# Kernel tuning notes

Measured on AMD Instinct MI355X. Metric: run time of the kernel, lower is better.

The kernel has to match this reference:

```python
import jax, jax.numpy as jnp
import numpy as np

PATCH = 96
VOL = 192
STRIDE = 48
C = 2
B = 1
GD = 48  # global low-res grid


def _gaussian_wt(p):
    # MONAI-style gaussian importance map: delta at center (p//2), sigma = 0.125*p,
    # separable gaussian product, normalized so max == 1.
    i = jnp.arange(p, dtype=jnp.float32)
    c = jnp.float32(p // 2)
    sigma = jnp.float32(0.125 * p)
    g = jnp.exp(-0.5 * ((i - c) / sigma) ** 2)
    w = g[:, None, None] * g[None, :, None] * g[None, None, :]  # [p,p,p]
    return w / w.max()


def setup_inputs() -> dict:
    key = jax.random.key(0)
    k1, k2 = jax.random.split(key)
    # deterministic overlapping patch grid (stride 48, patch 96, vol 192 -> 3 per axis)
    pos = list(range(0, VOL - PATCH + 1, STRIDE))
    starts = np.array([[d, h, w] for d in pos for h in pos for w in pos], dtype=np.int32)  # [27,3]
    K = starts.shape[0]
    patch_logits = jax.random.normal(k1, (K * B, C, PATCH, PATCH, PATCH), dtype=jnp.float32)
    global_logit = jax.random.normal(k2, (B, C, GD, GD, GD), dtype=jnp.float32)
    return {
        "patch_logits": patch_logits,
        "global_logit": global_logit,
        "patch_starts": jnp.asarray(starts),
    }


def reference(patch_logits, global_logit, patch_starts):
    K, Cc, P = patch_logits.shape[0], patch_logits.shape[1], patch_logits.shape[2]
    V = VOL
    wt = _gaussian_wt(P)  # [P,P,P], matches fixed_wt buffer

    offs = jnp.arange(P, dtype=jnp.int32)
    dd = patch_starts[:, 0][:, None] + offs  # [K,P]
    hh = patch_starts[:, 1][:, None] + offs
    ww = patch_starts[:, 2][:, None] + offs
    # flattened voxel index per patch element: [K,P,P,P]
    flat = ((dd[:, :, None, None] * V + hh[:, None, :, None]) * V + ww[:, None, None, :]).reshape(-1)

    # weighted scatter-add of all patches (batch=1 so all patches target batch 0)
    vals = (patch_logits * wt[None, None]).transpose(1, 0, 2, 3, 4).reshape(Cc, -1)  # [C, K*P^3]
    final = jnp.zeros((Cc, V * V * V), patch_logits.dtype).at[:, flat].add(vals)

    wvals = jnp.broadcast_to(wt, (K, P, P, P)).reshape(-1)
    wmap = jnp.full((V * V * V,), 1e-20, patch_logits.dtype).at[flat].add(wvals)
    mask = jnp.zeros((V * V * V,), patch_logits.dtype).at[flat].set(1.0)

    # trilinear upsample, align_corners=False (half-pixel) == jax.image.resize linear
    up = jax.image.resize(global_logit, (B, Cc, V, V, V), method='trilinear')

    out = (final / wmap).reshape(B, Cc, V, V, V)
    out = out + jnp.where(mask.reshape(B, 1, V, V, V) == 1.0, 0.0, up)
    return out
```

## Files before the change

### kernel.cpp

```cpp
#include <hip/hip_runtime.h>


constexpr int V  = 192;
constexpr int P  = 96;
constexpr int S  = 48;
constexpr int NC = 2;
constexpr int TH = 8;
constexpr int NT = 384;
constexpr int CF4 = TH * P / 4;
constexpr int NBLK = NC * V * (V / TH);

__global__ __launch_bounds__(NT) void
DynamicPatchAggregator_85418309583422_kernel(const float* __restrict__ patches,
                                             float* __restrict__ out)
{
    __shared__ __align__(16) float  sg[P];
    __shared__ __align__(16) float4 stage[12 * CF4];

    const int t = threadIdx.x;
    if (t < P) {
        float x = ((float)(t - 48)) * (1.0f / 12.0f);
        sg[t] = __expf(-0.5f * x * x);
    }

    const int bid = blockIdx.x;
    const int ht  = bid % (V / TH);
    const int d   = (bid / (V / TH)) % V;
    const int c   = bid / ((V / TH) * V);
    const int H0  = ht * TH;

    const int dq  = d / S;
    const int kd0 = max(0, dq - 1);
    const int nkd = (dq == 1 || dq == 2) ? 2 : 1;
    const int hq  = H0 / S;
    const int kh0 = max(0, hq - 1);
    const int nkh = (hq == 1 || hq == 2) ? 2 : 1;

    const int nchunk = nkd * nkh * 3;
    const int total  = nchunk * CF4;
    for (int base = t; base < total; base += 4 * NT) {
        float4 v[4];
        int   su[4];
        int nv = 0;
#pragma unroll
        for (int q = 0; q < 4; ++q) {
            const int u = base + q * NT;
            if (u < total) {
                const int chunk = u / CF4;
                const int r     = u % CF4;
                const int kw = chunk % 3;
                const int j  = (chunk / 3) % nkh;
                const int i  = chunk / (3 * nkh);
                const int kd = kd0 + i, kh = kh0 + j;
                const int pd  = d  - kd * S;
                const int ph0 = H0 - kh * S;
                const int k   = (kd * 3 + kh) * 3 + kw;
                const int off = (((k * NC + c) * P + pd) * P + ph0) * P;
                v[q]  = reinterpret_cast<const float4*>(patches + off)[r];
                su[q] = ((i * 2 + j) * 3 + kw) * CF4 + r;
                nv = q + 1;
            }
        }
#pragma unroll
        for (int q = 0; q < 4; ++q)
            if (q < nv) stage[su[q]] = v[q];
    }
    __syncthreads();

    const int hl = t / 48;
    const int w4 = t % 48;
    const int h  = H0 + hl;

    const int  wr  = w4 / 12;
    const int  kwa = max(0, wr - 1);
    const bool wv  = (wr == 1) | (wr == 2);
    const int  kwb = wv ? kwa + 1 : kwa;
    const int  pqa = w4 - kwa * 12;
    const int  pqb = wv ? pqa - 12 : pqa;
    const float4 gwa = reinterpret_cast<const float4*>(sg)[pqa];
    float4 gwb = reinterpret_cast<const float4*>(sg)[pqb];
    if (!wv) gwb = make_float4(0.0f, 0.0f, 0.0f, 0.0f);

    const float gd0 = sg[d - kd0 * S];
    const float gd1 = (nkd == 2) ? sg[d - (kd0 + 1) * S] : 0.0f;
    const float gh0 = sg[h - kh0 * S];
    const float gh1 = (nkh == 2) ? sg[h - (kh0 + 1) * S] : 0.0f;

    const float gdA[2] = {gd0, gd1};
    const float ghA[2] = {gh0, gh1};
    const int   iA[2]  = {0, nkd - 1};
    const int   jA[2]  = {0, nkh - 1};
    const int   kwA[2] = {kwa, kwb};
    const int   pqA[2] = {pqa, pqb};
    const float4 gwA[2] = {gwa, gwb};

    float4 acc = make_float4(0.0f, 0.0f, 0.0f, 0.0f);
#pragma unroll
    for (int i = 0; i < 2; ++i)
#pragma unroll
        for (int j = 0; j < 2; ++j) {
            const float a = gdA[i] * ghA[j];
#pragma unroll
            for (int k = 0; k < 2; ++k) {
                const float4 pv =
                    stage[((iA[i] * 2 + jA[j]) * 3 + kwA[k]) * CF4 + hl * 24 + pqA[k]];
                const float4 g = gwA[k];
                acc.x += (a * g.x) * pv.x;
                acc.y += (a * g.y) * pv.y;
                acc.z += (a * g.z) * pv.z;
                acc.w += (a * g.w) * pv.w;
            }
        }

    const float GdGh = (gd0 + gd1) * (gh0 + gh1);
    float4 o;
    o.x = acc.x / (GdGh * (gwa.x + gwb.x) + 1e-20f);
    o.y = acc.y / (GdGh * (gwa.y + gwb.y) + 1e-20f);
    o.z = acc.z / (GdGh * (gwa.z + gwb.z) + 1e-20f);
    o.w = acc.w / (GdGh * (gwa.w + gwb.w) + 1e-20f);

    reinterpret_cast<float4*>(out)[bid * NT + t] = o;
}

extern "C" void kernel_launch(void* const* d_in, const int* in_sizes, int n_in,
                              void* d_out, int out_size, void* d_ws, size_t ws_size,
                              hipStream_t stream) {
    const float* patches = (const float*)d_in[0];
    float* out = (float*)d_out;

    DynamicPatchAggregator_85418309583422_kernel<<<NBLK, NT, 0, stream>>>(patches, out);
}
```

Before: 309.6 us.

## Process six depth slices per block with double-buffered register-prefetch staging

Each block now covers six consecutive depth slices and four rows instead of one slice and eight rows. The next slice's patch data is loaded into registers while the current slice is computed, then committed to an alternate shared-memory buffer. Shared rows are padded to a stride of CF4+4. The aim is to hide global-load latency and to amortise block setup and Gaussian table computation across slices. In exchange the grid is much smaller, register pressure is higher (six float4 prefetch registers), and there is a barrier per slice.

```diff
diff --git a/kernel.cpp b/kernel.cpp
--- a/kernel.cpp
+++ b/kernel.cpp
@@ -1,21 +1,23 @@
 #include <hip/hip_runtime.h>
 
 
-constexpr int V  = 192;
-constexpr int P  = 96;
-constexpr int S  = 48;
-constexpr int NC = 2;
-constexpr int TH = 8;
-constexpr int NT = 384;
-constexpr int CF4 = TH * P / 4;
-constexpr int NBLK = NC * V * (V / TH);
+constexpr int V    = 192;
+constexpr int P    = 96;
+constexpr int S    = 48;
+constexpr int NC   = 2;
+constexpr int TH   = 4;
+constexpr int NT   = 192;
+constexpr int CF4  = TH * P / 4;
+constexpr int CSTR = CF4 + 4;
+constexpr int ND   = 6;
+constexpr int NBLK = NC * (V / ND) * (V / TH);
 
 __global__ __launch_bounds__(NT) void
 DynamicPatchAggregator_85418309583422_kernel(const float* __restrict__ patches,
                                              float* __restrict__ out)
 {
     __shared__ __align__(16) float  sg[P];
-    __shared__ __align__(16) float4 stage[12 * CF4];
+    __shared__ __align__(16) float4 stage[2][12 * CSTR];
 
     const int t = threadIdx.x;
     if (t < P) {
@@ -25,26 +27,39 @@
 
     const int bid = blockIdx.x;
     const int ht  = bid % (V / TH);
-    const int d   = (bid / (V / TH)) % V;
-    const int c   = bid / ((V / TH) * V);
+    const int dg  = (bid / (V / TH)) % (V / ND);
+    const int c   = bid / ((V / TH) * (V / ND));
     const int H0  = ht * TH;
+    const int d0  = dg * ND;
 
-    const int dq  = d / S;
+    const int dq  = d0 / S;
     const int kd0 = max(0, dq - 1);
     const int nkd = (dq == 1 || dq == 2) ? 2 : 1;
     const int hq  = H0 / S;
     const int kh0 = max(0, hq - 1);
     const int nkh = (hq == 1 || hq == 2) ? 2 : 1;
-
     const int nchunk = nkd * nkh * 3;
     const int total  = nchunk * CF4;
-    for (int base = t; base < total; base += 4 * NT) {
-        float4 v[4];
-        int   su[4];
-        int nv = 0;
+
+    const int hl = t / 48;
+    const int w4 = t % 48;
+    const int h  = H0 + hl;
+
+    const int  wr  = w4 / 12;
+    const int  kwa = max(0, wr - 1);
+    const bool wv  = (wr == 1) | (wr == 2);
+    const int  kwb = wv ? kwa + 1 : kwa;
+    const int  pqa = w4 - kwa * 12;
+    const int  pqb = wv ? pqa - 12 : pqa;
+
+    float4 v[6];
+    int    su[6];
+    int    nv = 0;
+    auto issue = [&](int d) {
+        nv = 0;
 #pragma unroll
-        for (int q = 0; q < 4; ++q) {
-            const int u = base + q * NT;
+        for (int q = 0; q < 6; ++q) {
+            const int u = t + q * NT;
             if (u < total) {
                 const int chunk = u / CF4;
                 const int r     = u % CF4;
@@ -57,69 +72,76 @@
                 const int k   = (kd * 3 + kh) * 3 + kw;
                 const int off = (((k * NC + c) * P + pd) * P + ph0) * P;
                 v[q]  = reinterpret_cast<const float4*>(patches + off)[r];
-                su[q] = ((i * 2 + j) * 3 + kw) * CF4 + r;
+                su[q] = ((i * 2 + j) * 3 + kw) * CSTR + r;
                 nv = q + 1;
             }
         }
+    };
+    auto commit = [&](int b) {
 #pragma unroll
-        for (int q = 0; q < 4; ++q)
-            if (q < nv) stage[su[q]] = v[q];
-    }
+        for (int q = 0; q < 6; ++q)
+            if (q < nv) stage[b][su[q]] = v[q];
+    };
+
+    issue(d0);
+    commit(0);
     __syncthreads();
 
-    const int hl = t / 48;
-    const int w4 = t % 48;
-    const int h  = H0 + hl;
-
-    const int  wr  = w4 / 12;
-    const int  kwa = max(0, wr - 1);
-    const bool wv  = (wr == 1) | (wr == 2);
-    const int  kwb = wv ? kwa + 1 : kwa;
-    const int  pqa = w4 - kwa * 12;
-    const int  pqb = wv ? pqa - 12 : pqa;
     const float4 gwa = reinterpret_cast<const float4*>(sg)[pqa];
     float4 gwb = reinterpret_cast<const float4*>(sg)[pqb];
     if (!wv) gwb = make_float4(0.0f, 0.0f, 0.0f, 0.0f);
-
-    const float gd0 = sg[d - kd0 * S];
-    const float gd1 = (nkd == 2) ? sg[d - (kd0 + 1) * S] : 0.0f;
     const float gh0 = sg[h - kh0 * S];
     const float gh1 = (nkh == 2) ? sg[h - (kh0 + 1) * S] : 0.0f;
+    const float Ghw0 = (gh0 + gh1);
 
-    const float gdA[2] = {gd0, gd1};
-    const float ghA[2] = {gh0, gh1};
     const int   iA[2]  = {0, nkd - 1};
     const int   jA[2]  = {0, nkh - 1};
     const int   kwA[2] = {kwa, kwb};
     const int   pqA[2] = {pqa, pqb};
-    const float4 gwA[2] = {gwa, gwb};
+    const float ghA[2] = {gh0, gh1};
 
-    float4 acc = make_float4(0.0f, 0.0f, 0.0f, 0.0f);
 #pragma unroll
-    for (int i = 0; i < 2; ++i)
+    for (int it = 0; it < ND; ++it) {
+        const int d   = d0 + it;
+        const int buf = it & 1;
+
+        if (it + 1 < ND) issue(d + 1);
+
+        const float gd0 = sg[d - kd0 * S];
+        const float gd1 = (nkd == 2) ? sg[d - (kd0 + 1) * S] : 0.0f;
+        const float gdA[2] = {gd0, gd1};
+
+        float4 acc = make_float4(0.0f, 0.0f, 0.0f, 0.0f);
 #pragma unroll
-        for (int j = 0; j < 2; ++j) {
-            const float a = gdA[i] * ghA[j];
+        for (int i = 0; i < 2; ++i)
 #pragma unroll
-            for (int k = 0; k < 2; ++k) {
-                const float4 pv =
-                    stage[((iA[i] * 2 + jA[j]) * 3 + kwA[k]) * CF4 + hl * 24 + pqA[k]];
-                const float4 g = gwA[k];
-                acc.x += (a * g.x) * pv.x;
-                acc.y += (a * g.y) * pv.y;
-                acc.z += (a * g.z) * pv.z;
-                acc.w += (a * g.w) * pv.w;
+            for (int j = 0; j < 2; ++j) {
+                const float a = gdA[i] * ghA[j];
+#pragma unroll
+                for (int k = 0; k < 2; ++k) {
+                    const float4 pv =
+                        stage[buf][((iA[i] * 2 + jA[j]) * 3 + kwA[k]) * CSTR + hl * 24 + pqA[k]];
+                    const float4 g = (k == 0) ? gwa : gwb;
+                    acc.x += (a * g.x) * pv.x;
+                    acc.y += (a * g.y) * pv.y;
+                    acc.z += (a * g.z) * pv.z;
+                    acc.w += (a * g.w) * pv.w;
+                }
             }
+
+        const float GdGh = (gd0 + gd1) * Ghw0;
+        float4 o;
+        o.x = acc.x / (GdGh * (gwa.x + gwb.x) + 1e-20f);
+        o.y = acc.y / (GdGh * (gwa.y + gwb.y) + 1e-20f);
+        o.z = acc.z / (GdGh * (gwa.z + gwb.z) + 1e-20f);
+        o.w = acc.w / (GdGh * (gwa.w + gwb.w) + 1e-20f);
+        reinterpret_cast<float4*>(out)[((c * V + d) * V + h) * 48 + w4] = o;
+
+        if (it + 1 < ND) {
+            commit(buf ^ 1);
+            __syncthreads();
         }
-
-    const float GdGh = (gd0 + gd1) * (gh0 + gh1);
-    float4 o;
-    o.x = acc.x / (GdGh * (gwa.x + gwb.x) + 1e-20f);
-    o.y = acc.y / (GdGh * (gwa.y + gwb.y) + 1e-20f);
-    o.z = acc.z / (GdGh * (gwa.z + gwb.z) + 1e-20f);
-    o.w = acc.w / (GdGh * (gwa.w + gwb.w) + 1e-20f);
-
-    reinterpret_cast<float4*>(out)[bid * NT + t] = o;
+    }
 }
 
 extern "C" void kernel_launch(void* const* d_in, const int* in_sizes, int n_in,
```

Result: slower. 347.6 us (+12.3%).
